# Kernel optimization log

Measured on AMD Instinct MI355X. Metric: run time of the kernel, lower is better.

Reference implementation:

```python
import jax, jax.numpy as jnp
import numpy as np

B, N, C, G = 8, 4096, 768, 16
D = C // G  # per-group channel dim = 48


def setup_inputs() -> dict:
    key = jax.random.key(0)
    ks = jax.random.split(key, 5)
    s = 1.0 / np.sqrt(C)
    return {
        "x": jax.random.normal(ks[0], (B, N, C), dtype=jnp.float32),
        "w_qkv": jax.random.normal(ks[1], (C, 3 * C), dtype=jnp.float32) * s,
        "b_qkv": jnp.zeros((3 * C,), dtype=jnp.float32),
        "w_proj": jax.random.normal(ks[2], (C, C), dtype=jnp.float32) * s,
        "b_proj": jnp.zeros((C,), dtype=jnp.float32),
    }


def reference(x, w_qkv, b_qkv, w_proj, b_proj):
    Bx, Nx, Cx = x.shape
    g, d = G, Cx // G
    qkv = x @ w_qkv + b_qkv                      # [B, N, 3C]
    qkv = qkv.reshape(Bx, Nx, 3, g, d)
    qkv = jnp.transpose(qkv, (2, 0, 3, 1, 4))    # [3, B, g, N, d]
    q, k, v = qkv[0], qkv[1], qkv[2]
    q = q * (float(Nx) ** -0.5)
    # channel attention: contract over tokens -> [B, g, d, d]
    attn = jnp.einsum("bgnd,bgne->bgde", q, k)
    attn = jax.nn.softmax(attn, axis=-1)
    # out = attn @ v^T -> [B, g, d, N], then back to [B, N, C]
    out = jnp.einsum("bgde,bgne->bgnd", attn, v)  # [B, g, N, d]
    out = jnp.transpose(out, (0, 2, 1, 3)).reshape(Bx, Nx, Cx)
    return out @ w_proj + b_proj
```

## Files before the change

kernel.cpp:

```cpp
#include <hip/hip_runtime.h>
#include <stdint.h>


using short8 = __attribute__((__ext_vector_type__(8))) short;
using f32x4  = __attribute__((__ext_vector_type__(4))) float;

typedef const void __attribute__((address_space(1))) gv_t;
typedef void __attribute__((address_space(3))) lv_t;

__device__ __forceinline__ void gll16(const void* g, void* l) {
  __builtin_amdgcn_global_load_lds((gv_t*)g, (lv_t*)l, 16, 0, 0);
}

__device__ __forceinline__ uint16_t f2b(float f) {
  uint32_t x = __float_as_uint(f);
  uint32_t r = (x + 0x7fffu + ((x >> 16) & 1u)) >> 16;
  return (uint16_t)r;
}
__device__ __forceinline__ float b2f(uint16_t u) {
  return __uint_as_float(((uint32_t)u) << 16);
}


__global__ __launch_bounds__(256) void cast_x_kernel(const float* __restrict__ x,
                                                     uint16_t* __restrict__ xb, int n4) {
  int i = blockIdx.x * 256 + threadIdx.x;
  if (i >= n4) return;
  f32x4 v = ((const f32x4*)x)[i];
  union { uint16_t u[4]; uint64_t q; } o;
  o.u[0] = f2b(v[0]); o.u[1] = f2b(v[1]); o.u[2] = f2b(v[2]); o.u[3] = f2b(v[3]);
  ((uint64_t*)xb)[i] = o.q;
}

__global__ __launch_bounds__(256) void transpose_cast_kernel(const float* __restrict__ w,
                                                             uint16_t* __restrict__ wt,
                                                             int K, int N) {
  int i = blockIdx.x * 256 + threadIdx.x;
  if (i >= N * K) return;
  int n = i / K, k = i - n * K;
  wt[i] = f2b(w[(size_t)k * N + n]);
}


__global__ __launch_bounds__(256, 2) void gemm_qkv_kernel(
    const uint16_t* __restrict__ A, const uint16_t* __restrict__ Bt,
    const float* __restrict__ bias,
    uint16_t* __restrict__ Qt, uint16_t* __restrict__ Kt, uint16_t* __restrict__ Vb) {
  __shared__ uint16_t As[128 * 32];
  __shared__ uint16_t Bs[128 * 32];
  const int tid = threadIdx.x;
  const int m0 = blockIdx.x * 128;
  const int n0 = blockIdx.y * 128;
  const int lane = tid & 63, wid = tid >> 6;
  const int wr = wid >> 1, wc = wid & 1;
  const int lrow = lane & 15, kb = lane >> 4;
  const int which = n0 / 768;
  const bool sw = (which < 2);

  const int off  = tid * 16;
  const int srow = off >> 6;
  const int scol = (off & 63) >> 1;

  f32x4 acc[4][4] = {};

  for (int k0 = 0; k0 < 768; k0 += 32) {
    gll16(A  + (size_t)(m0 + srow)      * 768 + k0 + scol, (char*)As + off);
    gll16(A  + (size_t)(m0 + 64 + srow) * 768 + k0 + scol, (char*)As + 4096 + off);
    gll16(Bt + (size_t)(n0 + srow)      * 768 + k0 + scol, (char*)Bs + off);
    gll16(Bt + (size_t)(n0 + 64 + srow) * 768 + k0 + scol, (char*)Bs + 4096 + off);
    __syncthreads();
    short8 av[4], bv[4];
#pragma unroll
    for (int m = 0; m < 4; ++m)
      av[m] = *(const short8*)(As + (wr * 64 + m * 16 + lrow) * 32 + kb * 8);
#pragma unroll
    for (int n = 0; n < 4; ++n)
      bv[n] = *(const short8*)(Bs + (wc * 64 + n * 16 + lrow) * 32 + kb * 8);
    if (sw) {
#pragma unroll
      for (int m = 0; m < 4; ++m)
#pragma unroll
        for (int n = 0; n < 4; ++n)
          acc[m][n] = __builtin_amdgcn_mfma_f32_16x16x32_bf16(bv[n], av[m], acc[m][n], 0, 0, 0);
    } else {
#pragma unroll
      for (int m = 0; m < 4; ++m)
#pragma unroll
        for (int n = 0; n < 4; ++n)
          acc[m][n] = __builtin_amdgcn_mfma_f32_16x16x32_bf16(av[m], bv[n], acc[m][n], 0, 0, 0);
    }
    __syncthreads();
  }

  const float qscale = 0.015625f;
  if (sw) {
    uint16_t* dst = (which == 0) ? Qt : Kt;
    const float sc = (which == 0) ? qscale : 1.0f;
#pragma unroll
    for (int m = 0; m < 4; ++m) {
      const int token = m0 + wr * 64 + m * 16 + lrow;
      const int b = token >> 12, nn = token & 4095;
#pragma unroll
      for (int n = 0; n < 4; ++n) {
        const int c0 = n0 - which * 768 + wc * 64 + n * 16 + kb * 4;
#pragma unroll
        for (int r = 0; r < 4; ++r) {
          const int chan = c0 + r;
          const int g = chan / 48;
          const int d = chan - g * 48;
          const float bvv = bias[n0 + wc * 64 + n * 16 + kb * 4 + r];
          dst[(((size_t)b * 16 + g) * 48 + d) * 4096 + nn] = f2b((acc[m][n][r] + bvv) * sc);
        }
      }
    }
  } else {
#pragma unroll
    for (int m = 0; m < 4; ++m) {
      const int row_b = m0 + wr * 64 + m * 16 + kb * 4;
#pragma unroll
      for (int n = 0; n < 4; ++n) {
        const int col = n0 + wc * 64 + n * 16 + lrow;
        const int c = col - 2 * 768;
        const int g = c / 48;
        const int d = c - g * 48;
        const float bv2 = bias[col];
#pragma unroll
        for (int r = 0; r < 4; ++r) {
          const int row = row_b + r;
          const int b = row >> 12, nn = row & 4095;
          Vb[(((size_t)b * 16 + g) * 4096 + nn) * 48 + d] = f2b(acc[m][n][r] + bv2);
        }
      }
    }
  }
}


__global__ __launch_bounds__(256) void logits_mfma_kernel(
    const uint16_t* __restrict__ Qt, const uint16_t* __restrict__ Kt,
    float* __restrict__ part) {
  const int bg = blockIdx.x;
  const int ch = blockIdx.y;
  const int tid = threadIdx.x;
  const int lane = tid & 63, w = tid >> 6;
  const int lrow = lane & 15, kb = lane >> 4;

  const size_t qbase = (size_t)bg * 48 * 4096;
  const int tok0 = ch * 512 + w * 128;

  f32x4 acc[3][3] = {};
#pragma unroll
  for (int s = 0; s < 4; ++s) {
    const int tok = tok0 + s * 32 + kb * 8;
    short8 av[3], bvv[3];
#pragma unroll
    for (int dm = 0; dm < 3; ++dm) {
      av[dm]  = *(const short8*)(Qt + qbase + (size_t)(dm * 16 + lrow) * 4096 + tok);
      bvv[dm] = *(const short8*)(Kt + qbase + (size_t)(dm * 16 + lrow) * 4096 + tok);
    }
#pragma unroll
    for (int dm = 0; dm < 3; ++dm)
#pragma unroll
      for (int em = 0; em < 3; ++em)
        acc[dm][em] = __builtin_amdgcn_mfma_f32_16x16x32_bf16(av[dm], bvv[em], acc[dm][em], 0, 0, 0);
  }

  __shared__ float red[4][2304];
#pragma unroll
  for (int dm = 0; dm < 3; ++dm)
#pragma unroll
    for (int em = 0; em < 3; ++em)
#pragma unroll
      for (int r = 0; r < 4; ++r) {
        const int d = dm * 16 + kb * 4 + r;
        const int e = em * 16 + lrow;
        red[w][d * 48 + e] = acc[dm][em][r];
      }
  __syncthreads();
  float* dst = part + ((size_t)ch * 128 + bg) * 2304;
  for (int i = tid; i < 2304; i += 256)
    dst[i] = red[0][i] + red[1][i] + red[2][i] + red[3][i];
}


__global__ __launch_bounds__(256) void softmax_kernel(const float* __restrict__ part,
                                                      float* __restrict__ attn) {
  const int bg = blockIdx.x;
  const int tid = threadIdx.x;
  __shared__ float l[2304];
  for (int p = tid; p < 2304; p += 256) {
    float s = 0.f;
    for (int chk = 0; chk < 8; ++chk) s += part[((size_t)chk * 128 + bg) * 2304 + p];
    l[p] = s;
  }
  __syncthreads();
  if (tid < 48) {
    const int d = tid;
    float m = -1e30f;
    for (int e = 0; e < 48; ++e) m = fmaxf(m, l[d * 48 + e]);
    float s = 0.f;
    for (int e = 0; e < 48; ++e) s += expf(l[d * 48 + e] - m);
    const float inv = 1.0f / s;
    for (int e = 0; e < 48; ++e)
      attn[(size_t)bg * 2304 + d * 48 + e] = expf(l[d * 48 + e] - m) * inv;
  }
}


__global__ __launch_bounds__(256) void blockdiag_kernel(const uint16_t* __restrict__ Vb,
                                                        const float* __restrict__ attn,
                                                        uint16_t* __restrict__ ao) {
  const int bg = blockIdx.x, ch = blockIdx.y;
  const int b = bg >> 4, g = bg & 15;
  const int tid = threadIdx.x;
  __shared__ uint16_t vs[128 * 64];
  __shared__ uint16_t as2[48 * 64];
  const size_t vbase = ((size_t)bg * 4096 + (size_t)ch * 128) * 48;
  for (int i = tid; i < 128 * 64; i += 256) {
    int n = i >> 6, e = i & 63;
    vs[i] = (e < 48) ? Vb[vbase + n * 48 + e] : (uint16_t)0;
  }
  const float* ab = attn + (size_t)bg * 2304;
  for (int i = tid; i < 48 * 64; i += 256) {
    int d = i >> 6, e = i & 63;
    as2[i] = (e < 48) ? f2b(ab[d * 48 + e]) : (uint16_t)0;
  }
  __syncthreads();
  const int lane = tid & 63, w = tid >> 6;
  const int lrow = lane & 15, kb = lane >> 4;
  f32x4 acc[2][3] = {};
#pragma unroll
  for (int ksb = 0; ksb < 2; ++ksb) {
    short8 a[2], bb[3];
#pragma unroll
    for (int i = 0; i < 2; ++i)
      a[i] = *(const short8*)(vs + (w * 32 + i * 16 + lrow) * 64 + ksb * 32 + kb * 8);
#pragma unroll
    for (int c = 0; c < 3; ++c)
      bb[c] = *(const short8*)(as2 + (c * 16 + lrow) * 64 + ksb * 32 + kb * 8);
#pragma unroll
    for (int i = 0; i < 2; ++i)
#pragma unroll
      for (int c = 0; c < 3; ++c)
        acc[i][c] = __builtin_amdgcn_mfma_f32_16x16x32_bf16(a[i], bb[c], acc[i][c], 0, 0, 0);
  }
#pragma unroll
  for (int i = 0; i < 2; ++i)
#pragma unroll
    for (int c = 0; c < 3; ++c)
#pragma unroll
      for (int r = 0; r < 4; ++r) {
        const int nl = w * 32 + i * 16 + kb * 4 + r;
        const int dcol = c * 16 + lrow;
        const size_t row = (size_t)b * 4096 + (size_t)ch * 128 + nl;
        ao[row * 768 + g * 48 + dcol] = f2b(acc[i][c][r]);
      }
}


__global__ __launch_bounds__(256, 2) void gemm_proj_kernel(
    const uint16_t* __restrict__ A, const uint16_t* __restrict__ Bt,
    const float* __restrict__ bias, float* __restrict__ out) {
  __shared__ uint16_t As[128 * 32];
  __shared__ uint16_t Bs[128 * 32];
  const int tid = threadIdx.x;
  const int m0 = blockIdx.x * 128;
  const int n0 = blockIdx.y * 128;
  const int lane = tid & 63, wid = tid >> 6;
  const int wr = wid >> 1, wc = wid & 1;
  const int lrow = lane & 15, kb = lane >> 4;

  const int off  = tid * 16;
  const int srow = off >> 6;
  const int scol = (off & 63) >> 1;

  f32x4 acc[4][4] = {};

  for (int k0 = 0; k0 < 768; k0 += 32) {
    gll16(A  + (size_t)(m0 + srow)      * 768 + k0 + scol, (char*)As + off);
    gll16(A  + (size_t)(m0 + 64 + srow) * 768 + k0 + scol, (char*)As + 4096 + off);
    gll16(Bt + (size_t)(n0 + srow)      * 768 + k0 + scol, (char*)Bs + off);
    gll16(Bt + (size_t)(n0 + 64 + srow) * 768 + k0 + scol, (char*)Bs + 4096 + off);
    __syncthreads();
    short8 av[4], bv[4];
#pragma unroll
    for (int m = 0; m < 4; ++m)
      av[m] = *(const short8*)(As + (wr * 64 + m * 16 + lrow) * 32 + kb * 8);
#pragma unroll
    for (int n = 0; n < 4; ++n)
      bv[n] = *(const short8*)(Bs + (wc * 64 + n * 16 + lrow) * 32 + kb * 8);
#pragma unroll
    for (int m = 0; m < 4; ++m)
#pragma unroll
      for (int n = 0; n < 4; ++n)
        acc[m][n] = __builtin_amdgcn_mfma_f32_16x16x32_bf16(av[m], bv[n], acc[m][n], 0, 0, 0);
    __syncthreads();
  }

#pragma unroll
  for (int m = 0; m < 4; ++m) {
    const int row_b = m0 + wr * 64 + m * 16 + kb * 4;
#pragma unroll
    for (int n = 0; n < 4; ++n) {
      const int col = n0 + wc * 64 + n * 16 + lrow;
      const float bv2 = bias[col];
#pragma unroll
      for (int r = 0; r < 4; ++r)
        out[(size_t)(row_b + r) * 768 + col] = acc[m][n][r] + bv2;
    }
  }
}


extern "C" void kernel_launch(void* const* d_in, const int* in_sizes, int n_in,
                              void* d_out, int out_size, void* d_ws, size_t ws_size,
                              hipStream_t stream) {
  const float* x      = (const float*)d_in[0];
  const float* w_qkv  = (const float*)d_in[1];
  const float* b_qkv  = (const float*)d_in[2];
  const float* w_proj = (const float*)d_in[3];
  const float* b_proj = (const float*)d_in[4];
  float* out = (float*)d_out;

  char* w = (char*)d_ws;
  uint16_t* xb  = (uint16_t*)w; w += (size_t)32768 * 768 * 2;
  uint16_t* wqT = (uint16_t*)w; w += (size_t)2304 * 768 * 2;
  uint16_t* wpT = (uint16_t*)w; w += (size_t)768 * 768 * 2;
  uint16_t* Qt  = (uint16_t*)w; w += (size_t)128 * 48 * 4096 * 2;
  uint16_t* Kt  = (uint16_t*)w; w += (size_t)128 * 48 * 4096 * 2;
  uint16_t* Vb  = (uint16_t*)w; w += (size_t)128 * 4096 * 48 * 2;
  float* part   = (float*)w;    w += (size_t)8 * 128 * 2304 * 4;
  float* attn   = (float*)w;    w += (size_t)128 * 2304 * 4;
  uint16_t* ao  = xb;

  cast_x_kernel<<<24576, 256, 0, stream>>>(x, xb, 6291456);
  transpose_cast_kernel<<<6912, 256, 0, stream>>>(w_qkv, wqT, 768, 2304);
  transpose_cast_kernel<<<2304, 256, 0, stream>>>(w_proj, wpT, 768, 768);
  gemm_qkv_kernel<<<dim3(256, 18), 256, 0, stream>>>(xb, wqT, b_qkv, Qt, Kt, Vb);
  logits_mfma_kernel<<<dim3(128, 8), 256, 0, stream>>>(Qt, Kt, part);
  softmax_kernel<<<128, 256, 0, stream>>>(part, attn);
  blockdiag_kernel<<<dim3(128, 32), 256, 0, stream>>>(Vb, attn, ao);
  gemm_proj_kernel<<<dim3(256, 6), 256, 0, stream>>>(ao, wpT, b_proj, out);
}
```

Measured before the change: 371.0 us.

## Replace both GEMMs with a pipelined 256x256 tiled kernel with LDS swizzle

Merges the QKV and projection GEMMs into one templated kernel with 256x256 tiles, 512 threads and a 4-stage ring of LDS buffers. Global-to-LDS loads run three k-steps ahead and are tracked with explicit vmcnt waits and a single barrier per step, replacing the old load-sync-compute-sync loop. It also XOR-swizzles the LDS layout to cut bank conflicts, remaps workgroup IDs so consecutive blocks are spread across 8 groups (likely for cache or XCD locality), and raises wave priority around the MFMA block. The cost is a much larger LDS footprint (128 KB per block) and higher register pressure from 32 accumulators per wave, which may limit occupancy.

```diff
diff --git a/kernel.cpp b/kernel.cpp
--- a/kernel.cpp
+++ b/kernel.cpp
@@ -42,94 +42,139 @@
 }
 
 
-__global__ __launch_bounds__(256, 2) void gemm_qkv_kernel(
+template<int MODE>
+__global__ __launch_bounds__(512, 2) void gemm256_kernel(
     const uint16_t* __restrict__ A, const uint16_t* __restrict__ Bt,
     const float* __restrict__ bias,
-    uint16_t* __restrict__ Qt, uint16_t* __restrict__ Kt, uint16_t* __restrict__ Vb) {
-  __shared__ uint16_t As[128 * 32];
-  __shared__ uint16_t Bs[128 * 32];
-  const int tid = threadIdx.x;
-  const int m0 = blockIdx.x * 128;
-  const int n0 = blockIdx.y * 128;
-  const int lane = tid & 63, wid = tid >> 6;
-  const int wr = wid >> 1, wc = wid & 1;
+    uint16_t* __restrict__ Qb, uint16_t* __restrict__ Kb,
+    uint16_t* __restrict__ Vb, float* __restrict__ outf) {
+  constexpr int NT = 24;
+  constexpr int NWG = (MODE == 0) ? 1152 : 384;
+  constexpr int CPX = NWG / 8;
+  __shared__ uint16_t lds[4 * 16384];
+
+  const int tid  = threadIdx.x;
+  const int lane = tid & 63, w = tid >> 6;
+  const int wm = w >> 2, wn = w & 3;
   const int lrow = lane & 15, kb = lane >> 4;
-  const int which = n0 / 768;
-  const bool sw = (which < 2);
-
-  const int off  = tid * 16;
-  const int srow = off >> 6;
-  const int scol = (off & 63) >> 1;
-
-  f32x4 acc[4][4] = {};
-
-  for (int k0 = 0; k0 < 768; k0 += 32) {
-    gll16(A  + (size_t)(m0 + srow)      * 768 + k0 + scol, (char*)As + off);
-    gll16(A  + (size_t)(m0 + 64 + srow) * 768 + k0 + scol, (char*)As + 4096 + off);
-    gll16(Bt + (size_t)(n0 + srow)      * 768 + k0 + scol, (char*)Bs + off);
-    gll16(Bt + (size_t)(n0 + 64 + srow) * 768 + k0 + scol, (char*)Bs + 4096 + off);
-    __syncthreads();
-    short8 av[4], bv[4];
-#pragma unroll
-    for (int m = 0; m < 4; ++m)
-      av[m] = *(const short8*)(As + (wr * 64 + m * 16 + lrow) * 32 + kb * 8);
-#pragma unroll
-    for (int n = 0; n < 4; ++n)
-      bv[n] = *(const short8*)(Bs + (wc * 64 + n * 16 + lrow) * 32 + kb * 8);
+
+  int wg = (int)blockIdx.x;
+  wg = (wg & 7) * CPX + (wg >> 3);
+  const int mblk = wg % 128, nblk = wg / 128;
+  const int m0 = mblk * 256, n0 = nblk * 256;
+  const bool sw = (MODE == 0) && (n0 < 1536);
+
+  const int grow  = lane >> 2;
+  const int gslot = ((lane & 3) ^ ((lane >> 3) & 3)) << 3;
+  const size_t arow0 = (size_t)(m0 + w * 32 + grow) * 768 + gslot;
+  const size_t brow0 = (size_t)(n0 + w * 32 + grow) * 768 + gslot;
+
+  auto stage = [&](int ts) {
+    const int sl = ts & 3;
+    const size_t ko = (size_t)ts * 32;
+    uint16_t* la = lds + sl * 16384 + w * 1024;
+    uint16_t* lb = la + 8192;
+    gll16(A  + arow0 + ko,            la);
+    gll16(A  + arow0 + ko + 16 * 768, la + 512);
+    gll16(Bt + brow0 + ko,            lb);
+    gll16(Bt + brow0 + ko + 16 * 768, lb + 512);
+  };
+
+  const int xslot = (kb ^ ((lrow >> 1) & 3)) << 3;
+
+  f32x4 acc[8][4] = {};
+
+  stage(0); stage(1); stage(2);
+  asm volatile("s_waitcnt vmcnt(8)" ::: "memory");
+  __builtin_amdgcn_s_barrier();
+  __builtin_amdgcn_sched_barrier(0);
+
+  for (int t = 0; t < NT; ++t) {
+    if (t + 3 < NT) stage(t + 3);
+    const uint16_t* sa = lds + (t & 3) * 16384;
+    const uint16_t* sb = sa + 8192;
+    short8 av[8], bv4[4];
+#pragma unroll
+    for (int mf = 0; mf < 8; ++mf)
+      av[mf] = *(const short8*)(sa + (wm * 128 + mf * 16 + lrow) * 32 + xslot);
+#pragma unroll
+    for (int nf = 0; nf < 4; ++nf)
+      bv4[nf] = *(const short8*)(sb + (wn * 64 + nf * 16 + lrow) * 32 + xslot);
+    __builtin_amdgcn_s_setprio(1);
     if (sw) {
 #pragma unroll
-      for (int m = 0; m < 4; ++m)
-#pragma unroll
-        for (int n = 0; n < 4; ++n)
-          acc[m][n] = __builtin_amdgcn_mfma_f32_16x16x32_bf16(bv[n], av[m], acc[m][n], 0, 0, 0);
+      for (int mf = 0; mf < 8; ++mf)
+#pragma unroll
+        for (int nf = 0; nf < 4; ++nf)
+          acc[mf][nf] = __builtin_amdgcn_mfma_f32_16x16x32_bf16(bv4[nf], av[mf], acc[mf][nf], 0, 0, 0);
     } else {
 #pragma unroll
-      for (int m = 0; m < 4; ++m)
-#pragma unroll
-        for (int n = 0; n < 4; ++n)
-          acc[m][n] = __builtin_amdgcn_mfma_f32_16x16x32_bf16(av[m], bv[n], acc[m][n], 0, 0, 0);
-    }
-    __syncthreads();
+      for (int mf = 0; mf < 8; ++mf)
+#pragma unroll
+        for (int nf = 0; nf < 4; ++nf)
+          acc[mf][nf] = __builtin_amdgcn_mfma_f32_16x16x32_bf16(av[mf], bv4[nf], acc[mf][nf], 0, 0, 0);
+    }
+    __builtin_amdgcn_s_setprio(0);
+    if (t < NT - 1) {
+      if (t <= NT - 4)      asm volatile("s_waitcnt vmcnt(8)" ::: "memory");
+      else if (t == NT - 3) asm volatile("s_waitcnt vmcnt(4)" ::: "memory");
+      else                  asm volatile("s_waitcnt vmcnt(0)" ::: "memory");
+      __builtin_amdgcn_s_barrier();
+      __builtin_amdgcn_sched_barrier(0);
+    }
   }
 
   const float qscale = 0.015625f;
-  if (sw) {
-    uint16_t* dst = (which == 0) ? Qt : Kt;
-    const float sc = (which == 0) ? qscale : 1.0f;
-#pragma unroll
-    for (int m = 0; m < 4; ++m) {
-      const int token = m0 + wr * 64 + m * 16 + lrow;
-      const int b = token >> 12, nn = token & 4095;
-#pragma unroll
-      for (int n = 0; n < 4; ++n) {
-        const int c0 = n0 - which * 768 + wc * 64 + n * 16 + kb * 4;
-#pragma unroll
-        for (int r = 0; r < 4; ++r) {
-          const int chan = c0 + r;
-          const int g = chan / 48;
-          const int d = chan - g * 48;
-          const float bvv = bias[n0 + wc * 64 + n * 16 + kb * 4 + r];
-          dst[(((size_t)b * 16 + g) * 48 + d) * 4096 + nn] = f2b((acc[m][n][r] + bvv) * sc);
+  if (MODE == 0) {
+    const int which = n0 / 768;
+    if (which < 2) {
+      uint16_t* dst = (which == 0) ? Qb : Kb;
+      const float sc = (which == 0) ? qscale : 1.0f;
+#pragma unroll
+      for (int mf = 0; mf < 8; ++mf) {
+        const int token = m0 + wm * 128 + mf * 16 + lrow;
+        const int b = token >> 12, nn = token & 4095;
+#pragma unroll
+        for (int nf = 0; nf < 4; ++nf) {
+          const int colb = n0 + wn * 64 + nf * 16 + kb * 4;
+#pragma unroll
+          for (int r = 0; r < 4; ++r) {
+            const int chan = colb + r - which * 768;
+            const int g = chan / 48, d = chan - g * 48;
+            dst[(((size_t)b * 16 + g) * 48 + d) * 4096 + nn] =
+                f2b((acc[mf][nf][r] + bias[colb + r]) * sc);
+          }
         }
       }
+    } else {
+#pragma unroll
+      for (int mf = 0; mf < 8; ++mf) {
+        const int rowb = m0 + wm * 128 + mf * 16 + kb * 4;
+#pragma unroll
+        for (int nf = 0; nf < 4; ++nf) {
+          const int col = n0 + wn * 64 + nf * 16 + lrow;
+          const int c = col - 1536, g = c / 48, d = c - g * 48;
+          const float bb = bias[col];
+#pragma unroll
+          for (int r = 0; r < 4; ++r) {
+            const int row = rowb + r;
+            const int b = row >> 12, nn = row & 4095;
+            Vb[(((size_t)b * 16 + g) * 4096 + nn) * 48 + d] = f2b(acc[mf][nf][r] + bb);
+          }
+        }
+      }
     }
   } else {
 #pragma unroll
-    for (int m = 0; m < 4; ++m) {
-      const int row_b = m0 + wr * 64 + m * 16 + kb * 4;
-#pragma unroll
-      for (int n = 0; n < 4; ++n) {
-        const int col = n0 + wc * 64 + n * 16 + lrow;
-        const int c = col - 2 * 768;
-        const int g = c / 48;
-        const int d = c - g * 48;
-        const float bv2 = bias[col];
-#pragma unroll
-        for (int r = 0; r < 4; ++r) {
-          const int row = row_b + r;
-          const int b = row >> 12, nn = row & 4095;
-          Vb[(((size_t)b * 16 + g) * 4096 + nn) * 48 + d] = f2b(acc[m][n][r] + bv2);
-        }
+    for (int mf = 0; mf < 8; ++mf) {
+      const int rowb = m0 + wm * 128 + mf * 16 + kb * 4;
+#pragma unroll
+      for (int nf = 0; nf < 4; ++nf) {
+        const int col = n0 + wn * 64 + nf * 16 + lrow;
+        const float bb = bias[col];
+#pragma unroll
+        for (int r = 0; r < 4; ++r)
+          outf[(size_t)(rowb + r) * 768 + col] = acc[mf][nf][r] + bb;
       }
     }
   }
@@ -258,60 +303,6 @@
 }
 
 
-__global__ __launch_bounds__(256, 2) void gemm_proj_kernel(
-    const uint16_t* __restrict__ A, const uint16_t* __restrict__ Bt,
-    const float* __restrict__ bias, float* __restrict__ out) {
-  __shared__ uint16_t As[128 * 32];
-  __shared__ uint16_t Bs[128 * 32];
-  const int tid = threadIdx.x;
-  const int m0 = blockIdx.x * 128;
-  const int n0 = blockIdx.y * 128;
-  const int lane = tid & 63, wid = tid >> 6;
-  const int wr = wid >> 1, wc = wid & 1;
-  const int lrow = lane & 15, kb = lane >> 4;
-
-  const int off  = tid * 16;
-  const int srow = off >> 6;
-  const int scol = (off & 63) >> 1;
-
-  f32x4 acc[4][4] = {};
-
-  for (int k0 = 0; k0 < 768; k0 += 32) {
-    gll16(A  + (size_t)(m0 + srow)      * 768 + k0 + scol, (char*)As + off);
-    gll16(A  + (size_t)(m0 + 64 + srow) * 768 + k0 + scol, (char*)As + 4096 + off);
-    gll16(Bt + (size_t)(n0 + srow)      * 768 + k0 + scol, (char*)Bs + off);
-    gll16(Bt + (size_t)(n0 + 64 + srow) * 768 + k0 + scol, (char*)Bs + 4096 + off);
-    __syncthreads();
-    short8 av[4], bv[4];
-#pragma unroll
-    for (int m = 0; m < 4; ++m)
-      av[m] = *(const short8*)(As + (wr * 64 + m * 16 + lrow) * 32 + kb * 8);
-#pragma unroll
-    for (int n = 0; n < 4; ++n)
-      bv[n] = *(const short8*)(Bs + (wc * 64 + n * 16 + lrow) * 32 + kb * 8);
-#pragma unroll
-    for (int m = 0; m < 4; ++m)
-#pragma unroll
-      for (int n = 0; n < 4; ++n)
-        acc[m][n] = __builtin_amdgcn_mfma_f32_16x16x32_bf16(av[m], bv[n], acc[m][n], 0, 0, 0);
-    __syncthreads();
-  }
-
-#pragma unroll
-  for (int m = 0; m < 4; ++m) {
-    const int row_b = m0 + wr * 64 + m * 16 + kb * 4;
-#pragma unroll
-    for (int n = 0; n < 4; ++n) {
-      const int col = n0 + wc * 64 + n * 16 + lrow;
-      const float bv2 = bias[col];
-#pragma unroll
-      for (int r = 0; r < 4; ++r)
-        out[(size_t)(row_b + r) * 768 + col] = acc[m][n][r] + bv2;
-    }
-  }
-}
-
-
 extern "C" void kernel_launch(void* const* d_in, const int* in_sizes, int n_in,
                               void* d_out, int out_size, void* d_ws, size_t ws_size,
                               hipStream_t stream) {
@@ -336,9 +327,9 @@
   cast_x_kernel<<<24576, 256, 0, stream>>>(x, xb, 6291456);
   transpose_cast_kernel<<<6912, 256, 0, stream>>>(w_qkv, wqT, 768, 2304);
   transpose_cast_kernel<<<2304, 256, 0, stream>>>(w_proj, wpT, 768, 768);
-  gemm_qkv_kernel<<<dim3(256, 18), 256, 0, stream>>>(xb, wqT, b_qkv, Qt, Kt, Vb);
+  gemm256_kernel<0><<<1152, 512, 0, stream>>>(xb, wqT, b_qkv, Qt, Kt, Vb, nullptr);
   logits_mfma_kernel<<<dim3(128, 8), 256, 0, stream>>>(Qt, Kt, part);
   softmax_kernel<<<128, 256, 0, stream>>>(part, attn);
   blockdiag_kernel<<<dim3(128, 32), 256, 0, stream>>>(Vb, attn, ao);
-  gemm_proj_kernel<<<dim3(256, 6), 256, 0, stream>>>(ao, wpT, b_proj, out);
-}
+  gemm256_kernel<1><<<384, 512, 0, stream>>>(ao, wpT, b_proj, nullptr, nullptr, nullptr, out);
+}
```

Measured after the change: 1.164 ms. 214% more time.

## Compute channel-attention logits via Gram matrix instead of materializing Q and K

Applied to the files above, without the earlier changes.

Rewrites the logits as Wq^T (X^T X) Wk plus bias correction terms, so Q and K are never materialized. A transposed bf16 copy of x is emitted during the cast, a per-batch 768x768 Gram matrix is built with split-K, and it is multiplied by the K weights and then the Q weights per group. The QKV GEMM shrinks to a V-only GEMM. The change also adds XCD-aware block swizzling and vectorized V loads in blockdiag. It trades about two thirds of the QKV GEMM FLOPs for smaller Gram GEMMs and extra launches, and rounds the Gram matrix and intermediate to bf16, which may change accuracy.

```diff
diff --git a/kernel.cpp b/kernel.cpp
--- a/kernel.cpp
+++ b/kernel.cpp
@@ -22,14 +22,37 @@
 }
 
 
-__global__ __launch_bounds__(256) void cast_x_kernel(const float* __restrict__ x,
-                                                     uint16_t* __restrict__ xb, int n4) {
-  int i = blockIdx.x * 256 + threadIdx.x;
-  if (i >= n4) return;
-  f32x4 v = ((const f32x4*)x)[i];
-  union { uint16_t u[4]; uint64_t q; } o;
-  o.u[0] = f2b(v[0]); o.u[1] = f2b(v[1]); o.u[2] = f2b(v[2]); o.u[3] = f2b(v[3]);
-  ((uint64_t*)xb)[i] = o.q;
+__global__ __launch_bounds__(256) void cast_xt_kernel(const float* __restrict__ x,
+                                                      uint16_t* __restrict__ xb,
+                                                      uint16_t* __restrict__ xt) {
+  __shared__ uint16_t lt[64 * 65];
+  const int b  = blockIdx.y;
+  const int tn = blockIdx.x & 63, tp = blockIdx.x >> 6;
+  const int n0 = tn * 64, p0 = tp * 64;
+  const int tid = threadIdx.x;
+  const int r = tid >> 2, cs = (tid & 3) << 4;
+
+  const size_t xrow = ((size_t)(b * 4096 + n0 + r)) * 768 + p0 + cs;
+  uint16_t v[16];
+#pragma unroll
+  for (int j = 0; j < 4; ++j) {
+    f32x4 f = *(const f32x4*)(x + xrow + 4 * j);
+#pragma unroll
+    for (int k = 0; k < 4; ++k) v[4 * j + k] = f2b(f[k]);
+  }
+  *(uint4*)(xb + xrow)     = *(const uint4*)&v[0];
+  *(uint4*)(xb + xrow + 8) = *(const uint4*)&v[8];
+#pragma unroll
+  for (int j = 0; j < 16; ++j) lt[r * 65 + cs + j] = v[j];
+  __syncthreads();
+
+  const int pr = tid >> 2, ns = (tid & 3) << 4;
+  uint16_t o[16];
+#pragma unroll
+  for (int j = 0; j < 16; ++j) o[j] = lt[(ns + j) * 65 + pr];
+  const size_t trow = ((size_t)(b * 768 + p0 + pr)) * 4096 + n0 + ns;
+  *(uint4*)(xt + trow)     = *(const uint4*)&o[0];
+  *(uint4*)(xt + trow + 8) = *(const uint4*)&o[8];
 }
 
 __global__ __launch_bounds__(256) void transpose_cast_kernel(const float* __restrict__ w,
@@ -42,32 +65,24 @@
 }
 
 
-__global__ __launch_bounds__(256, 2) void gemm_qkv_kernel(
-    const uint16_t* __restrict__ A, const uint16_t* __restrict__ Bt,
-    const float* __restrict__ bias,
-    uint16_t* __restrict__ Qt, uint16_t* __restrict__ Kt, uint16_t* __restrict__ Vb) {
-  __shared__ uint16_t As[128 * 32];
-  __shared__ uint16_t Bs[128 * 32];
-  const int tid = threadIdx.x;
-  const int m0 = blockIdx.x * 128;
-  const int n0 = blockIdx.y * 128;
+template<int NT>
+__device__ __forceinline__ void gemm2p_core(
+    const uint16_t* __restrict__ A, int lda,
+    const uint16_t* __restrict__ Bt, int ldb,
+    int m0, int n0, int tid, uint16_t* As, uint16_t* Bs, f32x4 (&acc)[4][4]) {
   const int lane = tid & 63, wid = tid >> 6;
   const int wr = wid >> 1, wc = wid & 1;
   const int lrow = lane & 15, kb = lane >> 4;
-  const int which = n0 / 768;
-  const bool sw = (which < 2);
-
   const int off  = tid * 16;
   const int srow = off >> 6;
   const int scol = (off & 63) >> 1;
 
-  f32x4 acc[4][4] = {};
-
-  for (int k0 = 0; k0 < 768; k0 += 32) {
-    gll16(A  + (size_t)(m0 + srow)      * 768 + k0 + scol, (char*)As + off);
-    gll16(A  + (size_t)(m0 + 64 + srow) * 768 + k0 + scol, (char*)As + 4096 + off);
-    gll16(Bt + (size_t)(n0 + srow)      * 768 + k0 + scol, (char*)Bs + off);
-    gll16(Bt + (size_t)(n0 + 64 + srow) * 768 + k0 + scol, (char*)Bs + 4096 + off);
+  for (int t = 0; t < NT; ++t) {
+    const int k0 = t * 32;
+    gll16(A  + (size_t)(m0 + srow)      * lda + k0 + scol, (char*)As + off);
+    gll16(A  + (size_t)(m0 + 64 + srow) * lda + k0 + scol, (char*)As + 4096 + off);
+    gll16(Bt + (size_t)(n0 + srow)      * ldb + k0 + scol, (char*)Bs + off);
+    gll16(Bt + (size_t)(n0 + 64 + srow) * ldb + k0 + scol, (char*)Bs + 4096 + off);
     __syncthreads();
     short8 av[4], bv[4];
 #pragma unroll
@@ -76,93 +91,193 @@
 #pragma unroll
     for (int n = 0; n < 4; ++n)
       bv[n] = *(const short8*)(Bs + (wc * 64 + n * 16 + lrow) * 32 + kb * 8);
-    if (sw) {
-#pragma unroll
-      for (int m = 0; m < 4; ++m)
-#pragma unroll
-        for (int n = 0; n < 4; ++n)
-          acc[m][n] = __builtin_amdgcn_mfma_f32_16x16x32_bf16(bv[n], av[m], acc[m][n], 0, 0, 0);
-    } else {
-#pragma unroll
-      for (int m = 0; m < 4; ++m)
-#pragma unroll
-        for (int n = 0; n < 4; ++n)
-          acc[m][n] = __builtin_amdgcn_mfma_f32_16x16x32_bf16(av[m], bv[n], acc[m][n], 0, 0, 0);
-    }
+#pragma unroll
+    for (int m = 0; m < 4; ++m)
+#pragma unroll
+      for (int n = 0; n < 4; ++n)
+        acc[m][n] = __builtin_amdgcn_mfma_f32_16x16x32_bf16(av[m], bv[n], acc[m][n], 0, 0, 0);
     __syncthreads();
   }
-
-  const float qscale = 0.015625f;
-  if (sw) {
-    uint16_t* dst = (which == 0) ? Qt : Kt;
-    const float sc = (which == 0) ? qscale : 1.0f;
-#pragma unroll
-    for (int m = 0; m < 4; ++m) {
-      const int token = m0 + wr * 64 + m * 16 + lrow;
-      const int b = token >> 12, nn = token & 4095;
-#pragma unroll
-      for (int n = 0; n < 4; ++n) {
-        const int c0 = n0 - which * 768 + wc * 64 + n * 16 + kb * 4;
-#pragma unroll
-        for (int r = 0; r < 4; ++r) {
-          const int chan = c0 + r;
-          const int g = chan / 48;
-          const int d = chan - g * 48;
-          const float bvv = bias[n0 + wc * 64 + n * 16 + kb * 4 + r];
-          dst[(((size_t)b * 16 + g) * 48 + d) * 4096 + nn] = f2b((acc[m][n][r] + bvv) * sc);
-        }
+}
+
+__device__ __forceinline__ int xcd_swizzle(int wg, int cpx) {
+  return (wg & 7) * cpx + (wg >> 3);
+}
+
+
+__global__ __launch_bounds__(256) void vgemm_kernel(
+    const uint16_t* __restrict__ A, const uint16_t* __restrict__ Bt,
+    const float* __restrict__ bias, uint16_t* __restrict__ Vb) {
+  __shared__ uint16_t As[128 * 32];
+  __shared__ uint16_t Bs[128 * 32];
+  const int tid = threadIdx.x;
+  int wg = xcd_swizzle((int)blockIdx.x, 1536 / 8);
+  const int mblk = wg / 6, nblk = wg % 6;
+  const int m0 = mblk * 128, n0 = nblk * 128;
+
+  f32x4 acc[4][4] = {};
+  gemm2p_core<24>(A, 768, Bt, 768, m0, n0, tid, As, Bs, acc);
+
+  const int lane = tid & 63, wid = tid >> 6;
+  const int wr = wid >> 1, wc = wid & 1;
+  const int lrow = lane & 15, kb = lane >> 4;
+#pragma unroll
+  for (int mf = 0; mf < 4; ++mf) {
+    const int rowb = m0 + wr * 64 + mf * 16 + kb * 4;
+#pragma unroll
+    for (int nf = 0; nf < 4; ++nf) {
+      const int c = n0 + wc * 64 + nf * 16 + lrow;
+      const int g = c / 48, d = c - g * 48;
+      const float bb = bias[1536 + c];
+#pragma unroll
+      for (int r = 0; r < 4; ++r) {
+        const int row = rowb + r;
+        const int b = row >> 12, nn = row & 4095;
+        Vb[(((size_t)b * 16 + g) * 4096 + nn) * 48 + d] = f2b(acc[mf][nf][r] + bb);
       }
     }
-  } else {
-#pragma unroll
-    for (int m = 0; m < 4; ++m) {
-      const int row_b = m0 + wr * 64 + m * 16 + kb * 4;
-#pragma unroll
-      for (int n = 0; n < 4; ++n) {
-        const int col = n0 + wc * 64 + n * 16 + lrow;
-        const int c = col - 2 * 768;
-        const int g = c / 48;
-        const int d = c - g * 48;
-        const float bv2 = bias[col];
-#pragma unroll
-        for (int r = 0; r < 4; ++r) {
-          const int row = row_b + r;
-          const int b = row >> 12, nn = row & 4095;
-          Vb[(((size_t)b * 16 + g) * 4096 + nn) * 48 + d] = f2b(acc[m][n][r] + bv2);
-        }
-      }
+  }
+}
+
+
+__global__ __launch_bounds__(256) void gram_kernel(const uint16_t* __restrict__ xt,
+                                                   float* __restrict__ G2) {
+  __shared__ uint16_t As[128 * 32];
+  __shared__ uint16_t Bs[128 * 32];
+  const int tid = threadIdx.x;
+  int wg = xcd_swizzle((int)blockIdx.x, 576 / 8);
+  const int b = wg / 72;
+  const int rem = wg % 72;
+  const int ks = rem / 36;
+  const int rr = rem % 36;
+  const int m0 = (rr / 6) * 128, n0 = (rr % 6) * 128;
+
+  const uint16_t* xtb = xt + (size_t)b * 768 * 4096 + (size_t)ks * 2048;
+  f32x4 acc[4][4] = {};
+  gemm2p_core<64>(xtb, 4096, xtb, 4096, m0, n0, tid, As, Bs, acc);
+
+  float* out = G2 + ((size_t)ks * 8 + b) * 589824;
+  const int lane = tid & 63, wid = tid >> 6;
+  const int wr = wid >> 1, wc = wid & 1;
+  const int lrow = lane & 15, kb = lane >> 4;
+#pragma unroll
+  for (int mf = 0; mf < 4; ++mf) {
+    const int rowb = m0 + wr * 64 + mf * 16 + kb * 4;
+#pragma unroll
+    for (int nf = 0; nf < 4; ++nf) {
+      const int col = n0 + wc * 64 + nf * 16 + lrow;
+#pragma unroll
+      for (int r = 0; r < 4; ++r)
+        out[(size_t)(rowb + r) * 768 + col] = acc[mf][nf][r];
     }
   }
 }
 
-
-__global__ __launch_bounds__(256) void logits_mfma_kernel(
-    const uint16_t* __restrict__ Qt, const uint16_t* __restrict__ Kt,
-    float* __restrict__ part) {
+__global__ __launch_bounds__(256) void reduceg_kernel(const float* __restrict__ G2,
+                                                      uint16_t* __restrict__ G) {
+  const size_t i = ((size_t)blockIdx.x * 256 + threadIdx.x) * 4;
+  f32x4 a = *(const f32x4*)(G2 + i);
+  f32x4 c = *(const f32x4*)(G2 + 4718592 + i);
+  uint16_t o[4];
+#pragma unroll
+  for (int j = 0; j < 4; ++j) o[j] = f2b(a[j] + c[j]);
+  *(uint64_t*)(G + i) = *(const uint64_t*)&o[0];
+}
+
+
+__global__ __launch_bounds__(256) void ttgemm_kernel(const uint16_t* __restrict__ wkT,
+                                                     const uint16_t* __restrict__ G,
+                                                     uint16_t* __restrict__ Tt) {
+  __shared__ uint16_t As[128 * 32];
+  __shared__ uint16_t Bs[128 * 32];
+  const int tid = threadIdx.x;
+  int wg = xcd_swizzle((int)blockIdx.x, 288 / 8);
+  const int b = wg / 36;
+  const int rr = wg % 36;
+  const int m0 = (rr / 6) * 128, n0 = (rr % 6) * 128;
+
+  const uint16_t* Gb = G + (size_t)b * 589824;
+  f32x4 acc[4][4] = {};
+  gemm2p_core<24>(wkT, 768, Gb, 768, m0, n0, tid, As, Bs, acc);
+
+  uint16_t* out = Tt + (size_t)b * 589824;
+  const int lane = tid & 63, wid = tid >> 6;
+  const int wr = wid >> 1, wc = wid & 1;
+  const int lrow = lane & 15, kb = lane >> 4;
+#pragma unroll
+  for (int mf = 0; mf < 4; ++mf) {
+    const int rowb = m0 + wr * 64 + mf * 16 + kb * 4;
+#pragma unroll
+    for (int nf = 0; nf < 4; ++nf) {
+      const int col = n0 + wc * 64 + nf * 16 + lrow;
+#pragma unroll
+      for (int r = 0; r < 4; ++r)
+        out[(size_t)(rowb + r) * 768 + col] = f2b(acc[mf][nf][r]);
+    }
+  }
+}
+
+
+__global__ __launch_bounds__(256) void sb_kernel(const uint16_t* __restrict__ xt,
+                                                 float* __restrict__ s) {
+  const int j = blockIdx.x * 256 + threadIdx.x;
+  const uint16_t* row = xt + (size_t)j * 4096;
+  float acc = 0.f;
+  for (int i = 0; i < 4096; i += 8) {
+    short8 v = *(const short8*)(row + i);
+#pragma unroll
+    for (int k = 0; k < 8; ++k) acc += b2f((uint16_t)v[k]);
+  }
+  s[j] = acc;
+}
+
+
+__global__ __launch_bounds__(256) void sw_kernel(const float* __restrict__ s,
+                                                 const uint16_t* __restrict__ wqT,
+                                                 float* __restrict__ swv) {
+  __shared__ float sl[768];
+  const int b = blockIdx.x / 6, cblk = blockIdx.x % 6;
+  const int tid = threadIdx.x;
+  for (int i = tid; i < 768; i += 256) sl[i] = s[b * 768 + i];
+  __syncthreads();
+  const int c = cblk * 256 + tid;
+  const uint16_t* wr = wqT + (size_t)c * 768;
+  float acc = 0.f;
+  for (int p = 0; p < 768; p += 8) {
+    short8 v = *(const short8*)(wr + p);
+#pragma unroll
+    for (int k = 0; k < 8; ++k) acc += sl[p + k] * b2f((uint16_t)v[k]);
+  }
+  swv[b * 1536 + c] = acc;
+}
+
+
+__global__ __launch_bounds__(256) void logits48_kernel(
+    const uint16_t* __restrict__ wqT, const uint16_t* __restrict__ Tt,
+    const float* __restrict__ swv, const float* __restrict__ bqkv,
+    float* __restrict__ attn) {
   const int bg = blockIdx.x;
-  const int ch = blockIdx.y;
+  const int b = bg >> 4, g = bg & 15;
   const int tid = threadIdx.x;
   const int lane = tid & 63, w = tid >> 6;
   const int lrow = lane & 15, kb = lane >> 4;
 
-  const size_t qbase = (size_t)bg * 48 * 4096;
-  const int tok0 = ch * 512 + w * 128;
-
+  const uint16_t* ttb = Tt + (size_t)b * 589824;
   f32x4 acc[3][3] = {};
 #pragma unroll
-  for (int s = 0; s < 4; ++s) {
-    const int tok = tok0 + s * 32 + kb * 8;
-    short8 av[3], bvv[3];
+  for (int s = 0; s < 6; ++s) {
+    const int p = w * 192 + s * 32 + kb * 8;
+    short8 av[3], bv[3];
 #pragma unroll
     for (int dm = 0; dm < 3; ++dm) {
-      av[dm]  = *(const short8*)(Qt + qbase + (size_t)(dm * 16 + lrow) * 4096 + tok);
-      bvv[dm] = *(const short8*)(Kt + qbase + (size_t)(dm * 16 + lrow) * 4096 + tok);
+      av[dm] = *(const short8*)(wqT + (size_t)(g * 48 + dm * 16 + lrow) * 768 + p);
+      bv[dm] = *(const short8*)(ttb + (size_t)(g * 48 + dm * 16 + lrow) * 768 + p);
     }
 #pragma unroll
     for (int dm = 0; dm < 3; ++dm)
 #pragma unroll
       for (int em = 0; em < 3; ++em)
-        acc[dm][em] = __builtin_amdgcn_mfma_f32_16x16x32_bf16(av[dm], bvv[em], acc[dm][em], 0, 0, 0);
+        acc[dm][em] = __builtin_amdgcn_mfma_f32_16x16x32_bf16(av[dm], bv[em], acc[dm][em], 0, 0, 0);
   }
 
   __shared__ float red[4][2304];
@@ -177,32 +292,25 @@
         red[w][d * 48 + e] = acc[dm][em][r];
       }
   __syncthreads();
-  float* dst = part + ((size_t)ch * 128 + bg) * 2304;
-  for (int i = tid; i < 2304; i += 256)
-    dst[i] = red[0][i] + red[1][i] + red[2][i] + red[3][i];
-}
-
-
-__global__ __launch_bounds__(256) void softmax_kernel(const float* __restrict__ part,
-                                                      float* __restrict__ attn) {
-  const int bg = blockIdx.x;
-  const int tid = threadIdx.x;
-  __shared__ float l[2304];
-  for (int p = tid; p < 2304; p += 256) {
-    float s = 0.f;
-    for (int chk = 0; chk < 8; ++chk) s += part[((size_t)chk * 128 + bg) * 2304 + p];
-    l[p] = s;
+  for (int i = tid; i < 2304; i += 256) {
+    float v = red[0][i] + red[1][i] + red[2][i] + red[3][i];
+    const int d = i / 48, e = i - d * 48;
+    const float bq = bqkv[g * 48 + d];
+    const float bk = bqkv[768 + g * 48 + e];
+    v += bq * swv[b * 1536 + 768 + g * 48 + e] + bk * swv[b * 1536 + g * 48 + d]
+         + 4096.f * bq * bk;
+    red[0][i] = v * 0.015625f;
   }
   __syncthreads();
   if (tid < 48) {
     const int d = tid;
     float m = -1e30f;
-    for (int e = 0; e < 48; ++e) m = fmaxf(m, l[d * 48 + e]);
-    float s = 0.f;
-    for (int e = 0; e < 48; ++e) s += expf(l[d * 48 + e] - m);
-    const float inv = 1.0f / s;
+    for (int e = 0; e < 48; ++e) m = fmaxf(m, red[0][d * 48 + e]);
+    float ssum = 0.f;
+    for (int e = 0; e < 48; ++e) ssum += expf(red[0][d * 48 + e] - m);
+    const float inv = 1.0f / ssum;
     for (int e = 0; e < 48; ++e)
-      attn[(size_t)bg * 2304 + d * 48 + e] = expf(l[d * 48 + e] - m) * inv;
+      attn[(size_t)bg * 2304 + d * 48 + e] = expf(red[0][d * 48 + e] - m) * inv;
   }
 }
 
@@ -216,9 +324,15 @@
   __shared__ uint16_t vs[128 * 64];
   __shared__ uint16_t as2[48 * 64];
   const size_t vbase = ((size_t)bg * 4096 + (size_t)ch * 128) * 48;
-  for (int i = tid; i < 128 * 64; i += 256) {
-    int n = i >> 6, e = i & 63;
-    vs[i] = (e < 48) ? Vb[vbase + n * 48 + e] : (uint16_t)0;
+  const uint4* vg = (const uint4*)(Vb + vbase);
+  for (int u = tid; u < 768; u += 256) {
+    const int n = u / 6, c = u - n * 6;
+    *(uint4*)(vs + n * 64 + c * 8) = vg[u];
+  }
+  {
+    const int n = tid >> 1, c = 6 + (tid & 1);
+    uint4 z; z.x = z.y = z.z = z.w = 0u;
+    *(uint4*)(vs + n * 64 + c * 8) = z;
   }
   const float* ab = attn + (size_t)bg * 2304;
   for (int i = tid; i < 48 * 64; i += 256) {
@@ -258,55 +372,32 @@
 }
 
 
-__global__ __launch_bounds__(256, 2) void gemm_proj_kernel(
+__global__ __launch_bounds__(256) void projgemm_kernel(
     const uint16_t* __restrict__ A, const uint16_t* __restrict__ Bt,
     const float* __restrict__ bias, float* __restrict__ out) {
   __shared__ uint16_t As[128 * 32];
   __shared__ uint16_t Bs[128 * 32];
   const int tid = threadIdx.x;
-  const int m0 = blockIdx.x * 128;
-  const int n0 = blockIdx.y * 128;
+  int wg = xcd_swizzle((int)blockIdx.x, 1536 / 8);
+  const int mblk = wg / 6, nblk = wg % 6;
+  const int m0 = mblk * 128, n0 = nblk * 128;
+
+  f32x4 acc[4][4] = {};
+  gemm2p_core<24>(A, 768, Bt, 768, m0, n0, tid, As, Bs, acc);
+
   const int lane = tid & 63, wid = tid >> 6;
   const int wr = wid >> 1, wc = wid & 1;
   const int lrow = lane & 15, kb = lane >> 4;
-
-  const int off  = tid * 16;
-  const int srow = off >> 6;
-  const int scol = (off & 63) >> 1;
-
-  f32x4 acc[4][4] = {};
-
-  for (int k0 = 0; k0 < 768; k0 += 32) {
-    gll16(A  + (size_t)(m0 + srow)      * 768 + k0 + scol, (char*)As + off);
-    gll16(A  + (size_t)(m0 + 64 + srow) * 768 + k0 + scol, (char*)As + 4096 + off);
-    gll16(Bt + (size_t)(n0 + srow)      * 768 + k0 + scol, (char*)Bs + off);
-    gll16(Bt + (size_t)(n0 + 64 + srow) * 768 + k0 + scol, (char*)Bs + 4096 + off);
-    __syncthreads();
-    short8 av[4], bv[4];
-#pragma unroll
-    for (int m = 0; m < 4; ++m)
-      av[m] = *(const short8*)(As + (wr * 64 + m * 16 + lrow) * 32 + kb * 8);
-#pragma unroll
-    for (int n = 0; n < 4; ++n)
-      bv[n] = *(const short8*)(Bs + (wc * 64 + n * 16 + lrow) * 32 + kb * 8);
-#pragma unroll
-    for (int m = 0; m < 4; ++m)
-#pragma unroll
-      for (int n = 0; n < 4; ++n)
-        acc[m][n] = __builtin_amdgcn_mfma_f32_16x16x32_bf16(av[m], bv[n], acc[m][n], 0, 0, 0);
-    __syncthreads();
-  }
-
-#pragma unroll
-  for (int m = 0; m < 4; ++m) {
-    const int row_b = m0 + wr * 64 + m * 16 + kb * 4;
-#pragma unroll
-    for (int n = 0; n < 4; ++n) {
-      const int col = n0 + wc * 64 + n * 16 + lrow;
-      const float bv2 = bias[col];
+#pragma unroll
+  for (int mf = 0; mf < 4; ++mf) {
+    const int rowb = m0 + wr * 64 + mf * 16 + kb * 4;
+#pragma unroll
+    for (int nf = 0; nf < 4; ++nf) {
+      const int col = n0 + wc * 64 + nf * 16 + lrow;
+      const float bb = bias[col];
 #pragma unroll
       for (int r = 0; r < 4; ++r)
-        out[(size_t)(row_b + r) * 768 + col] = acc[m][n][r] + bv2;
+        out[(size_t)(rowb + r) * 768 + col] = acc[mf][nf][r] + bb;
     }
   }
 }
@@ -326,19 +417,26 @@
   uint16_t* xb  = (uint16_t*)w; w += (size_t)32768 * 768 * 2;
   uint16_t* wqT = (uint16_t*)w; w += (size_t)2304 * 768 * 2;
   uint16_t* wpT = (uint16_t*)w; w += (size_t)768 * 768 * 2;
-  uint16_t* Qt  = (uint16_t*)w; w += (size_t)128 * 48 * 4096 * 2;
-  uint16_t* Kt  = (uint16_t*)w; w += (size_t)128 * 48 * 4096 * 2;
+  uint16_t* xt  = (uint16_t*)w; w += (size_t)8 * 768 * 4096 * 2;
   uint16_t* Vb  = (uint16_t*)w; w += (size_t)128 * 4096 * 48 * 2;
-  float* part   = (float*)w;    w += (size_t)8 * 128 * 2304 * 4;
-  float* attn   = (float*)w;    w += (size_t)128 * 2304 * 4;
+  float*    G2  = (float*)w;    w += (size_t)2 * 8 * 768 * 768 * 4;
+  uint16_t* G   = (uint16_t*)w; w += (size_t)8 * 768 * 768 * 2;
+  uint16_t* Tt  = (uint16_t*)w; w += (size_t)8 * 768 * 768 * 2;
+  float*    s   = (float*)w;    w += (size_t)8 * 768 * 4;
+  float*    swv = (float*)w;    w += (size_t)8 * 1536 * 4;
+  float*    attn= (float*)w;    w += (size_t)128 * 2304 * 4;
   uint16_t* ao  = xb;
 
-  cast_x_kernel<<<24576, 256, 0, stream>>>(x, xb, 6291456);
+  cast_xt_kernel<<<dim3(768, 8), 256, 0, stream>>>(x, xb, xt);
   transpose_cast_kernel<<<6912, 256, 0, stream>>>(w_qkv, wqT, 768, 2304);
   transpose_cast_kernel<<<2304, 256, 0, stream>>>(w_proj, wpT, 768, 768);
-  gemm_qkv_kernel<<<dim3(256, 18), 256, 0, stream>>>(xb, wqT, b_qkv, Qt, Kt, Vb);
-  logits_mfma_kernel<<<dim3(128, 8), 256, 0, stream>>>(Qt, Kt, part);
-  softmax_kernel<<<128, 256, 0, stream>>>(part, attn);
+  vgemm_kernel<<<1536, 256, 0, stream>>>(xb, wqT + (size_t)1536 * 768, b_qkv, Vb);
+  gram_kernel<<<576, 256, 0, stream>>>(xt, G2);
+  reduceg_kernel<<<4608, 256, 0, stream>>>(G2, G);
+  sb_kernel<<<24, 256, 0, stream>>>(xt, s);
+  sw_kernel<<<48, 256, 0, stream>>>(s, wqT, swv);
+  ttgemm_kernel<<<288, 256, 0, stream>>>(wqT + (size_t)768 * 768, G, Tt);
+  logits48_kernel<<<128, 256, 0, stream>>>(wqT, Tt, swv, b_qkv, attn);
   blockdiag_kernel<<<dim3(128, 32), 256, 0, stream>>>(Vb, attn, ao);
-  gemm_proj_kernel<<<dim3(256, 6), 256, 0, stream>>>(ao, wpT, b_proj, out);
-}
+  projgemm_kernel<<<1536, 256, 0, stream>>>(ao, wpT, b_proj, out);
+}
```

Measured after the change: 400.9 us. +8.1%, slower.
